# Optimization experiments

Hardware: AMD Instinct MI355X
Metric: run time of the kernel (lower is better)

Reference implementation:

```python
import jax, jax.numpy as jnp
import numpy as np
import math

N = 50000
E = 800000
NFEAT = 128
NLABEL = 8
H = 8        # nhead (hard-coded to 8 in __init__)
C = 32       # per-head channels (nhid arg)
HC = H * C   # 256, effective nhid after GAT concat
FDIM = HC + NLABEL  # 264
TDIM = 128


def sinusoidal_pos_emb(t, num_steps, dim, rescale=4):
    # x / num_steps * num_steps * rescale == x * rescale (kept faithful)
    xs = t / num_steps * num_steps * rescale
    half = dim // 2
    freqs = jnp.exp(jnp.arange(half, dtype=jnp.float32) * (-math.log(10000.0) / (half - 1)))
    ang = xs[:, None] * freqs[None, :]
    return jnp.concatenate([jnp.sin(ang), jnp.cos(ang)], axis=-1)


def gat_layer(h_in, W, a_src, a_dst, b, src, dst, n):
    # h_in: [N, Fin]; W: [Fin, H*C]; a_src/a_dst: [H, C]; b: [H*C]
    h = (h_in @ W).reshape(n, H, C)
    alpha_s = jnp.einsum('nhc,hc->nh', h, a_src)  # [N,H]
    alpha_d = jnp.einsum('nhc,hc->nh', h, a_dst)
    e = jax.nn.leaky_relu(alpha_s[src] + alpha_d[dst], 0.2)  # [E,H]
    # segment softmax over incoming edges of each destination node
    e = e - jax.ops.segment_max(e, dst, num_segments=n)[dst]
    ex = jnp.exp(e)
    denom = jax.ops.segment_sum(ex, dst, num_segments=n)[dst]
    alpha = ex / denom
    msg = h[src] * alpha[:, :, None]               # [E,H,C]
    out = jax.ops.segment_sum(msg, dst, num_segments=n)  # [N,H,C]
    return out.reshape(n, HC) + b


def setup_inputs() -> dict:
    key = jax.random.key(0)
    ks = jax.random.split(key, 24)
    s = 0.05
    inp = {
        'x': jax.random.normal(ks[0], (N, NFEAT), dtype=jnp.float32),
        'q_Y_sample': jax.random.normal(ks[1], (N, NLABEL), dtype=jnp.float32),
        'adj': jax.random.randint(ks[2], (2, E), 0, N, dtype=jnp.int64),
        't': jax.random.uniform(ks[3], (1,), dtype=jnp.float32) * 1000.0,
        'num_steps': 1000,
        # GAT layer params (layer 0 has different input dim)
        'W0': jax.random.normal(ks[4], (NFEAT + NLABEL, HC), dtype=jnp.float32) * s,
        'W1': jax.random.normal(ks[5], (HC + NLABEL, HC), dtype=jnp.float32) * s,
        'W2': jax.random.normal(ks[6], (HC + NLABEL, HC), dtype=jnp.float32) * s,
        'att_src': jax.random.normal(ks[7], (3, H, C), dtype=jnp.float32) * s,
        'att_dst': jax.random.normal(ks[8], (3, H, C), dtype=jnp.float32) * s,
        'bias': jax.random.normal(ks[9], (3, HC), dtype=jnp.float32) * s,
        # time MLP: Linear(128,128) -> ELU -> Linear(128, HC)
        'tmlp_w1': jax.random.normal(ks[10], (TDIM, TDIM), dtype=jnp.float32) * s,
        'tmlp_b1': jnp.zeros((TDIM,), dtype=jnp.float32),
        'tmlp_w2': jax.random.normal(ks[11], (TDIM, HC), dtype=jnp.float32) * s,
        'tmlp_b2': jnp.zeros((HC,), dtype=jnp.float32),
        # final MLP: fdim -> 2*fdim -> nlabel, ELU between, no BN
        'fin_w1': jax.random.normal(ks[12], (FDIM, 2 * FDIM), dtype=jnp.float32) * s,
        'fin_b1': jnp.zeros((2 * FDIM,), dtype=jnp.float32),
        'fin_w2': jax.random.normal(ks[13], (2 * FDIM, NLABEL), dtype=jnp.float32) * s,
        'fin_b2': jnp.zeros((NLABEL,), dtype=jnp.float32),
    }
    return inp


def reference(x, q_Y_sample, adj, t, num_steps, W0, W1, W2, att_src, att_dst, bias,
              tmlp_w1, tmlp_b1, tmlp_w2, tmlp_b2, fin_w1, fin_b1, fin_w2, fin_b2):
    n = x.shape[0]
    # time embedding -> [1, HC]
    temb = sinusoidal_pos_emb(t, num_steps, TDIM)
    temb = jax.nn.elu(temb @ tmlp_w1 + tmlp_b1) @ tmlp_w2 + tmlp_b2
    # edge index with self-loops (PyG GATConv add_self_loops=True)
    loops = jnp.arange(n)
    src = jnp.concatenate([adj[0], loops])
    dst = jnp.concatenate([adj[1], loops])
    h = jnp.concatenate([x, q_Y_sample], axis=-1)
    Ws = (W0, W1, W2)
    for i in range(3):
        conv = gat_layer(h, Ws[i], att_src[i], att_dst[i], bias[i], src, dst, n)
        h = jax.nn.elu(conv + temb)          # ELU activation (GATConv branch)
        h = jnp.concatenate([h, q_Y_sample], axis=-1)
    # final MLP
    return jax.nn.elu(h @ fin_w1 + fin_b1) @ fin_w2 + fin_b2
```

## Files before the change

### kernel.cpp

```cpp
#include <hip/hip_runtime.h>
#include <math.h>

#define N_NODES 50000
#define NE      800000
#define NEL     (NE + N_NODES)
#define NL      8
#define LDHB    288
#define KP0     160
#define KP1     288
#define NBLK    196
#define EDGEBLK ((NEL + 255) / 256)
#define HB_BLKS ((N_NODES * 36 + 255) / 256)
#define TR_BLKS 97

typedef __attribute__((ext_vector_type(8))) short bf16x8;
typedef __attribute__((ext_vector_type(4))) float f32x4;

__device__ __forceinline__ float elu_f(float x) { return x > 0.f ? x : __expf(x) - 1.f; }
__device__ __forceinline__ float bl(unsigned u) { return __uint_as_float(u << 16); }
__device__ __forceinline__ float bh(unsigned u) { return __uint_as_float(u & 0xffff0000u); }
__device__ __forceinline__ unsigned short f2b(float f) {
    unsigned u = __float_as_uint(f);
    u += 0x7fff + ((u >> 16) & 1);
    return (unsigned short)(u >> 16);
}
__device__ __forceinline__ unsigned pk2(float lo, float hi) {
    return (unsigned)f2b(lo) | ((unsigned)f2b(hi) << 16);
}
__device__ __forceinline__ int xcd_swizzle(int b, int nwg) {
    int q = nwg >> 3, r = nwg & 7;
    int xcd = b & 7, idx = b >> 3;
    return (xcd < r ? xcd * (q + 1) : r * (q + 1) + (xcd - r) * q) + idx;
}

__global__ void prep_kernel(const float* __restrict__ x, const float* __restrict__ q,
                            unsigned short* __restrict__ hbuf,
                            const float* __restrict__ W0, const float* __restrict__ W1,
                            const float* __restrict__ W2, const float* __restrict__ fw1,
                            unsigned short* __restrict__ wt0, unsigned short* __restrict__ wt1,
                            unsigned short* __restrict__ wt2, unsigned short* __restrict__ fw1t,
                            const int* __restrict__ adj, int* __restrict__ deg,
                            const float* __restrict__ t, const int* __restrict__ nst,
                            const float* __restrict__ tw1, const float* __restrict__ tb1,
                            const float* __restrict__ tw2, const float* __restrict__ tb2,
                            float* __restrict__ temb) {
    __shared__ float tlds[64][65];
    int bid = blockIdx.x, tid = threadIdx.x;
    if (bid < HB_BLKS) {
        int item = bid * 256 + tid;
        if (item >= N_NODES * 36) return;
        int n = item / 36, g = item - n * 36;
        float4 a = make_float4(0.f, 0.f, 0.f, 0.f), b = a;
        if (g < 16) {
            a = *(const float4*)(x + (size_t)n * 128 + g * 8);
            b = *(const float4*)(x + (size_t)n * 128 + g * 8 + 4);
        } else if (g == 16 || g == 32) {
            a = *(const float4*)(q + (size_t)n * 8);
            b = *(const float4*)(q + (size_t)n * 8 + 4);
        }
        uint4 o = make_uint4(pk2(a.x, a.y), pk2(a.z, a.w), pk2(b.x, b.y), pk2(b.z, b.w));
        *(uint4*)(hbuf + (size_t)n * LDHB + g * 8) = o;
        return;
    }
    int j = bid - HB_BLKS;
    if (j < TR_BLKS) {
        const float* W; unsigned short* WT; int K, NN, Kpad, nt;
        if (j < 12)      { W = W0;  WT = wt0;  K = 136; NN = 256; Kpad = KP0; nt = 4; }
        else if (j < 32) { W = W1;  WT = wt1;  K = 264; NN = 256; Kpad = KP1; nt = 4; j -= 12; }
        else if (j < 52) { W = W2;  WT = wt2;  K = 264; NN = 256; Kpad = KP1; nt = 4; j -= 32; }
        else             { W = fw1; WT = fw1t; K = 264; NN = 528; Kpad = KP1; nt = 9; j -= 52; }
        int tk = j / nt, tn = j - tk * nt;
        for (int i = tid; i < 4096; i += 256) {
            int r = i >> 6, c = i & 63;
            int k = tk * 64 + r, n = tn * 64 + c;
            tlds[r][c] = (k < K && n < NN) ? W[(size_t)k * NN + n] : 0.f;
        }
        __syncthreads();
        for (int i = tid; i < 4096; i += 256) {
            int r = i >> 6, c = i & 63;
            int n = tn * 64 + r, kp = tk * 64 + c;
            if (n < NN && kp < Kpad) WT[(size_t)n * Kpad + kp] = f2b(tlds[c][r]);
        }
        return;
    }
    j -= TR_BLKS;
    if (j < EDGEBLK) {
        int e = j * 256 + tid;
        if (e >= NEL) return;
        int d = (e < NE) ? adj[NE + e] : (e - NE);
        atomicAdd(&deg[d], 1);
        return;
    }
    __shared__ float emb[128];
    __shared__ float h1[128];
    float tv = t[0];
    float ns = (float)nst[0];
    float xs = tv / ns * ns * 4.0f;
    if (tid < 64) {
        float fr  = expf((float)tid * (-logf(10000.f) / 63.f));
        float ang = xs * fr;
        emb[tid]      = sinf(ang);
        emb[tid + 64] = cosf(ang);
    }
    __syncthreads();
    if (tid < 128) {
        float a = tb1[tid];
        for (int i = 0; i < 128; ++i) a += emb[i] * tw1[i * 128 + tid];
        h1[tid] = elu_f(a);
    }
    __syncthreads();
    float a = tb2[tid];
    for (int jj = 0; jj < 128; ++jj) a += h1[jj] * tw2[jj * 256 + tid];
    temb[tid] = a;
}

__global__ void scan1_kernel(const int* __restrict__ deg, int* __restrict__ excl,
                             int* __restrict__ bsum) {
    __shared__ int wsum[4];
    int idx = blockIdx.x * 256 + threadIdx.x;
    int lane = threadIdx.x & 63, wid = threadIdx.x >> 6;
    int v = (idx < N_NODES) ? deg[idx] : 0;
    int x = v;
#pragma unroll
    for (int off = 1; off < 64; off <<= 1) {
        int tv2 = __shfl_up(x, off);
        if (lane >= off) x += tv2;
    }
    if (lane == 63) wsum[wid] = x;
    __syncthreads();
    int woff = 0;
    for (int w = 0; w < wid; ++w) woff += wsum[w];
    if (idx < N_NODES) excl[idx] = woff + x - v;
    if (threadIdx.x == 255) bsum[blockIdx.x] = woff + x;
}

__global__ void scan2_kernel(int* __restrict__ bsum, int* __restrict__ boff) {
    __shared__ int wsum[4];
    int tid = threadIdx.x;
    int lane = tid & 63, wid = tid >> 6;
    int v = (tid < NBLK) ? bsum[tid] : 0;
    int x = v;
#pragma unroll
    for (int off = 1; off < 64; off <<= 1) {
        int tv2 = __shfl_up(x, off);
        if (lane >= off) x += tv2;
    }
    if (lane == 63) wsum[wid] = x;
    __syncthreads();
    int woff = 0;
    for (int w = 0; w < wid; ++w) woff += wsum[w];
    if (tid < NBLK) boff[tid] = woff + x - v;
}

__global__ void scan3_kernel(const int* __restrict__ excl, const int* __restrict__ boff,
                             int* __restrict__ rowptr, int* __restrict__ wptr) {
    int idx = blockIdx.x * 256 + threadIdx.x;
    if (idx < N_NODES) {
        int r = excl[idx] + boff[idx >> 8];
        rowptr[idx] = r;
        wptr[idx] = r;
    }
    if (idx == 0) rowptr[N_NODES] = NEL;
}

__global__ void scatter_kernel(const int* __restrict__ adj, int* __restrict__ wptr,
                               int* __restrict__ srcs) {
    int e = blockIdx.x * 256 + threadIdx.x;
    if (e >= NEL) return;
    int s, d;
    if (e < NE) { s = adj[e]; d = adj[NE + e]; }
    else        { s = d = e - NE; }
    int pos = atomicAdd(&wptr[d], 1);
    srcs[pos] = s;
}

template<int NK>
__device__ __forceinline__ void gemm_mainloop(
    const unsigned short* __restrict__ A, int lda,
    const unsigned short* __restrict__ Bt, int ldb,
    int M, int NCm1, int row0, int col0,
    char* lds, f32x4 (&acc)[4][4]) {
    int tid = threadIdx.x;
    int l = tid & 63, w = tid >> 6;
    int wr = w >> 1, wc = w & 1;
    int lr = l & 15, lq = l >> 4;

    int rr0 = w * 16 + (l >> 2);
    int rr1 = 64 + rr0;
    int kg0 = (l & 3) ^ ((rr0 >> 1) & 3);
    int kg1 = (l & 3) ^ ((rr1 >> 1) & 3);
    const unsigned short* gA0 = A + (size_t)min(row0 + rr0, M - 1) * lda + kg0 * 8;
    const unsigned short* gA1 = A + (size_t)min(row0 + rr1, M - 1) * lda + kg1 * 8;
    const unsigned short* gB0 = Bt + (size_t)min(col0 + rr0, NCm1) * ldb + kg0 * 8;
    const unsigned short* gB1 = Bt + (size_t)min(col0 + rr1, NCm1) * ldb + kg1 * 8;
    int la0 = w * 1024;
    int la1 = 4096 + w * 1024;

    int swz = ((lq ^ ((lr >> 1) & 3)) << 4);
    int abase = (wr * 64 + lr) * 64 + swz;
    int bbase = (wc * 64 + lr) * 64 + swz;

#define STAGE(buf, ks)                                                                  \
    {                                                                                   \
        char* base_ = lds + (buf) * 16384;                                              \
        __builtin_amdgcn_global_load_lds(                                               \
            (const __attribute__((address_space(1))) unsigned*)(gA0 + (ks) * 32),       \
            (__attribute__((address_space(3))) unsigned*)(base_ + la0), 16, 0, 0);      \
        __builtin_amdgcn_global_load_lds(                                               \
            (const __attribute__((address_space(1))) unsigned*)(gA1 + (ks) * 32),       \
            (__attribute__((address_space(3))) unsigned*)(base_ + la1), 16, 0, 0);      \
        __builtin_amdgcn_global_load_lds(                                               \
            (const __attribute__((address_space(1))) unsigned*)(gB0 + (ks) * 32),       \
            (__attribute__((address_space(3))) unsigned*)(base_ + 8192 + la0), 16, 0, 0);\
        __builtin_amdgcn_global_load_lds(                                               \
            (const __attribute__((address_space(1))) unsigned*)(gB1 + (ks) * 32),       \
            (__attribute__((address_space(3))) unsigned*)(base_ + 8192 + la1), 16, 0, 0);\
    }

    STAGE(0, 0);
    int cur = 0;
#pragma unroll
    for (int ks = 0; ks < NK; ++ks) {
        if (ks + 1 < NK) {
            STAGE(cur ^ 1, ks + 1);
            asm volatile("s_waitcnt vmcnt(4)" ::: "memory");
        } else {
            asm volatile("s_waitcnt vmcnt(0)" ::: "memory");
        }
        __builtin_amdgcn_s_barrier();
        char* Asc = lds + cur * 16384;
        char* Bsc = Asc + 8192;
        bf16x8 af[4], bfr[4];
#pragma unroll
        for (int m = 0; m < 4; ++m) af[m]  = *(const bf16x8*)(Asc + abase + m * 1024);
#pragma unroll
        for (int n = 0; n < 4; ++n) bfr[n] = *(const bf16x8*)(Bsc + bbase + n * 1024);
#pragma unroll
        for (int m = 0; m < 4; ++m)
#pragma unroll
            for (int n = 0; n < 4; ++n)
                acc[m][n] = __builtin_amdgcn_mfma_f32_16x16x32_bf16(af[m], bfr[n], acc[m][n], 0, 0, 0);
        asm volatile("s_waitcnt lgkmcnt(0)" ::: "memory");
        __builtin_amdgcn_s_barrier();
        cur ^= 1;
    }
#undef STAGE
}

template<int NK>
__global__ __launch_bounds__(256) void layer_gemm_kernel(
    const unsigned short* __restrict__ A, int lda,
    const unsigned short* __restrict__ Bt, int ldb,
    unsigned short* __restrict__ C, int M,
    const float* __restrict__ asrc, const float* __restrict__ adst,
    float* __restrict__ alpha_s, float* __restrict__ alpha_d) {
    __shared__ char lds[2][16384];
    int wg = xcd_swizzle(blockIdx.x, gridDim.x);
    int row0 = (wg >> 1) * 128, col0 = (wg & 1) * 128;
    int lane = threadIdx.x & 63, w = threadIdx.x >> 6;
    int wr = w >> 1, wc = w & 1;
    int lr = lane & 15, lq = lane >> 4;

    f32x4 acc[4][4];
#pragma unroll
    for (int m = 0; m < 4; ++m)
#pragma unroll
        for (int n = 0; n < 4; ++n) acc[m][n] = (f32x4){0.f, 0.f, 0.f, 0.f};

    gemm_mainloop<NK>(A, lda, Bt, ldb, M, 255, row0, col0, &lds[0][0], acc);

    float asv[4], adv[4];
#pragma unroll
    for (int n = 0; n < 4; ++n) {
        int c = col0 + wc * 64 + n * 16 + lr;
        asv[n] = asrc[c];
        adv[n] = adst[c];
    }
    int h0 = (col0 >> 5) + wc * 2;
    float* aptr = (lr & 2) ? alpha_d : alpha_s;
    int hsel = h0 + (lr & 1);

#pragma unroll
    for (int m = 0; m < 4; ++m) {
        int rbase = row0 + wr * 64 + m * 16 + lq * 4;
#pragma unroll
        for (int i = 0; i < 4; ++i) {
            int row = rbase + i;
            float pAs = acc[m][0][i] * asv[0] + acc[m][1][i] * asv[1];
            float pBs = acc[m][2][i] * asv[2] + acc[m][3][i] * asv[3];
            float pAd = acc[m][0][i] * adv[0] + acc[m][1][i] * adv[1];
            float pBd = acc[m][2][i] * adv[2] + acc[m][3][i] * adv[3];
            float ks_ = (lr & 1) ? pBs : pAs, ss = (lr & 1) ? pAs : pBs;
            float kd_ = (lr & 1) ? pBd : pAd, sd = (lr & 1) ? pAd : pBd;
            float vs = ks_ + __shfl_xor(ss, 1);
            float vd = kd_ + __shfl_xor(sd, 1);
            float kv = (lr & 2) ? vd : vs, sv = (lr & 2) ? vs : vd;
            float vv = kv + __shfl_xor(sv, 2);
            vv += __shfl_xor(vv, 4);
            vv += __shfl_xor(vv, 8);
            if (row < M) {
                if (lr < 4) aptr[row * NL + hsel] = vv;
#pragma unroll
                for (int n = 0; n < 4; ++n) {
                    int col = col0 + wc * 64 + n * 16 + lr;
                    C[(size_t)row * 256 + col] = f2b(acc[m][n][i]);
                }
            }
        }
    }
}

template<int NK>
__global__ __launch_bounds__(256) void fin_gemm_kernel(
    const unsigned short* __restrict__ A, int lda,
    const unsigned short* __restrict__ Bt, int ldb,
    int M, const float* __restrict__ fb1, const float* __restrict__ w2,
    float* __restrict__ partial) {
    __shared__ char lds[2][16384];
    int wg = xcd_swizzle(blockIdx.x, gridDim.x);
    int by = wg % 5, bx = wg / 5;
    int row0 = bx * 128, col0 = by * 128;
    int lane = threadIdx.x & 63, w = threadIdx.x >> 6;
    int wr = w >> 1, wc = w & 1;
    int lr = lane & 15, lq = lane >> 4;

    f32x4 acc[4][4];
#pragma unroll
    for (int m = 0; m < 4; ++m)
#pragma unroll
        for (int n = 0; n < 4; ++n) acc[m][n] = (f32x4){0.f, 0.f, 0.f, 0.f};

    gemm_mainloop<NK>(A, lda, Bt, ldb, M, 527, row0, col0, &lds[0][0], acc);

    float fbv[4], w2v[4][8];
#pragma unroll
    for (int n = 0; n < 4; ++n) {
        int c = col0 + wc * 64 + n * 16 + lr;
        if (c < 528) {
            fbv[n] = fb1[c];
            float4 wlo = *(const float4*)(w2 + (size_t)c * 8);
            float4 whi = *(const float4*)(w2 + (size_t)c * 8 + 4);
            w2v[n][0] = wlo.x; w2v[n][1] = wlo.y; w2v[n][2] = wlo.z; w2v[n][3] = wlo.w;
            w2v[n][4] = whi.x; w2v[n][5] = whi.y; w2v[n][6] = whi.z; w2v[n][7] = whi.w;
        } else {
            fbv[n] = 0.f;
#pragma unroll
            for (int j = 0; j < 8; ++j) w2v[n][j] = 0.f;
        }
    }
    int jsel = ((lr & 1) << 2) | (lr & 2) | ((lr >> 2) & 1);

    float* pbase = partial + (size_t)(by * 2 + wc) * N_NODES * 8;
#pragma unroll
    for (int m = 0; m < 4; ++m) {
        int rbase = row0 + wr * 64 + m * 16 + lq * 4;
#pragma unroll
        for (int i = 0; i < 4; ++i) {
            int row = rbase + i;
            float pj[8];
#pragma unroll
            for (int j = 0; j < 8; ++j) pj[j] = 0.f;
#pragma unroll
            for (int n = 0; n < 4; ++n) {
                float v = elu_f(acc[m][n][i] + fbv[n]);
#pragma unroll
                for (int j = 0; j < 8; ++j) pj[j] += v * w2v[n][j];
            }
            float v4[4];
#pragma unroll
            for (int j2 = 0; j2 < 4; ++j2) {
                float keep = (lr & 1) ? pj[j2 + 4] : pj[j2];
                float send = (lr & 1) ? pj[j2] : pj[j2 + 4];
                v4[j2] = keep + __shfl_xor(send, 1);
            }
            float v2[2];
#pragma unroll
            for (int j2 = 0; j2 < 2; ++j2) {
                float keep = (lr & 2) ? v4[j2 + 2] : v4[j2];
                float send = (lr & 2) ? v4[j2] : v4[j2 + 2];
                v2[j2] = keep + __shfl_xor(send, 2);
            }
            float keep = (lr & 4) ? v2[1] : v2[0];
            float send = (lr & 4) ? v2[0] : v2[1];
            float v1 = keep + __shfl_xor(send, 4);
            v1 += __shfl_xor(v1, 8);
            if (lr < 8 && row < M) pbase[(size_t)row * 8 + jsel] = v1;
        }
    }
}

__global__ void reduce_kernel(const float* __restrict__ partial, const float* __restrict__ fb2,
                              float* __restrict__ out) {
    int idx = blockIdx.x * 256 + threadIdx.x;
    if (idx >= N_NODES * NL) return;
    float a = fb2[idx & 7];
#pragma unroll
    for (int p = 0; p < 10; ++p) a += partial[(size_t)p * N_NODES * 8 + idx];
    out[idx] = a;
}

__global__ __launch_bounds__(256) void gather_kernel(
    const int* __restrict__ rowptr, const int* __restrict__ srcs,
    const float* __restrict__ alpha_s, const float* __restrict__ alpha_d,
    const unsigned short* __restrict__ hproj, const float* __restrict__ bias,
    const float* __restrict__ temb, unsigned short* __restrict__ h) {
    int node = blockIdx.x * 4 + (threadIdx.x >> 6);
    int lane = threadIdx.x & 63;
    int half = lane >> 5;
    int l32  = lane & 31;
    int hd   = l32 >> 2;
    float ad = alpha_d[node * NL + hd];
    int beg = rowptr[node], end = rowptr[node + 1];
    const uint4* hp4 = (const uint4*)hproj;
    float ac0[8], ac1[8];
#pragma unroll
    for (int j = 0; j < 8; ++j) { ac0[j] = 0.f; ac1[j] = 0.f; }
    float den0 = 0.f, den1 = 0.f;
    int i = beg + half;
    for (; i + 2 < end; i += 4) {
        int sA = srcs[i], sB = srcs[i + 2];
        float aA = alpha_s[sA * NL + hd] + ad;
        float aB = alpha_s[sB * NL + hd] + ad;
        aA = aA > 0.f ? aA : 0.2f * aA;
        aB = aB > 0.f ? aB : 0.2f * aB;
        float eA = __expf(aA);
        float eB = __expf(aB);
        uint4 hA = hp4[(size_t)sA * 32 + l32];
        uint4 hB = hp4[(size_t)sB * 32 + l32];
        ac0[0] += eA * bl(hA.x); ac0[1] += eA * bh(hA.x);
        ac0[2] += eA * bl(hA.y); ac0[3] += eA * bh(hA.y);
        ac0[4] += eA * bl(hA.z); ac0[5] += eA * bh(hA.z);
        ac0[6] += eA * bl(hA.w); ac0[7] += eA * bh(hA.w);
        den0 += eA;
        ac1[0] += eB * bl(hB.x); ac1[1] += eB * bh(hB.x);
        ac1[2] += eB * bl(hB.y); ac1[3] += eB * bh(hB.y);
        ac1[4] += eB * bl(hB.z); ac1[5] += eB * bh(hB.z);
        ac1[6] += eB * bl(hB.w); ac1[7] += eB * bh(hB.w);
        den1 += eB;
    }
    for (; i < end; i += 2) {
        int sA = srcs[i];
        float aA = alpha_s[sA * NL + hd] + ad;
        aA = aA > 0.f ? aA : 0.2f * aA;
        float eA = __expf(aA);
        uint4 hA = hp4[(size_t)sA * 32 + l32];
        ac0[0] += eA * bl(hA.x); ac0[1] += eA * bh(hA.x);
        ac0[2] += eA * bl(hA.y); ac0[3] += eA * bh(hA.y);
        ac0[4] += eA * bl(hA.z); ac0[5] += eA * bh(hA.z);
        ac0[6] += eA * bl(hA.w); ac0[7] += eA * bh(hA.w);
        den0 += eA;
    }
    float den = den0 + den1;
    den += __shfl_xor(den, 32);
    float av[8];
#pragma unroll
    for (int j = 0; j < 8; ++j) {
        av[j] = ac0[j] + ac1[j];
        av[j] += __shfl_xor(av[j], 32);
    }
    if (half == 0) {
        float inv = 1.f / den;
        int c = l32 * 8;
        float4 b0 = *(const float4*)(bias + c);
        float4 b1 = *(const float4*)(bias + c + 4);
        float4 t0 = *(const float4*)(temb + c);
        float4 t1 = *(const float4*)(temb + c + 4);
        uint4 o;
        o.x = pk2(elu_f(av[0] * inv + b0.x + t0.x), elu_f(av[1] * inv + b0.y + t0.y));
        o.y = pk2(elu_f(av[2] * inv + b0.z + t0.z), elu_f(av[3] * inv + b0.w + t0.w));
        o.z = pk2(elu_f(av[4] * inv + b1.x + t1.x), elu_f(av[5] * inv + b1.y + t1.y));
        o.w = pk2(elu_f(av[6] * inv + b1.z + t1.z), elu_f(av[7] * inv + b1.w + t1.w));
        *(uint4*)&h[(size_t)node * LDHB + c] = o;
    }
}

extern "C" void kernel_launch(void* const* d_in, const int* in_sizes, int n_in,
                              void* d_out, int out_size, void* d_ws, size_t ws_size,
                              hipStream_t stream) {
    const float* x   = (const float*)d_in[0];
    const float* q   = (const float*)d_in[1];
    const int*   adj = (const int*)d_in[2];
    const float* t   = (const float*)d_in[3];
    const int*   nst = (const int*)d_in[4];
    const float* W0  = (const float*)d_in[5];
    const float* W1  = (const float*)d_in[6];
    const float* W2  = (const float*)d_in[7];
    const float* att_src = (const float*)d_in[8];
    const float* att_dst = (const float*)d_in[9];
    const float* bias    = (const float*)d_in[10];
    const float* tw1 = (const float*)d_in[11];
    const float* tb1 = (const float*)d_in[12];
    const float* tw2 = (const float*)d_in[13];
    const float* tb2 = (const float*)d_in[14];
    const float* fw1 = (const float*)d_in[15];
    const float* fb1 = (const float*)d_in[16];
    const float* fw2 = (const float*)d_in[17];
    const float* fb2 = (const float*)d_in[18];
    float* out = (float*)d_out;

    char* ws = (char*)d_ws;
    unsigned short* hbuf = (unsigned short*)ws;
    char* p = ws + (size_t)N_NODES * LDHB * 2;
    unsigned short* hproj = (unsigned short*)p;  p += (size_t)N_NODES * 256 * 2;
    float* partial = (float*)p;                  p += (size_t)10 * N_NODES * 8 * 4;
    float* temb    = (float*)p;                  p += 1024;
    float* alpha_s = (float*)p;                  p += (size_t)N_NODES * NL * 4;
    float* alpha_d = (float*)p;                  p += (size_t)N_NODES * NL * 4;
    unsigned short* wt0  = (unsigned short*)p;   p += (size_t)256 * KP0 * 2;
    unsigned short* wt1  = (unsigned short*)p;   p += (size_t)256 * KP1 * 2;
    unsigned short* wt2  = (unsigned short*)p;   p += (size_t)256 * KP1 * 2;
    unsigned short* fw1t = (unsigned short*)p;   p += (size_t)528 * KP1 * 2;
    int* deg    = (int*)p;                       p += (size_t)N_NODES * 4;
    int* excl   = (int*)p;                       p += (size_t)N_NODES * 4;
    int* bsum   = (int*)p;                       p += 1024;
    int* boff   = (int*)p;                       p += 1024;
    int* rowptr = (int*)p;                       p += (size_t)(N_NODES + 4) * 4;
    int* wptr   = (int*)p;                       p += (size_t)N_NODES * 4;
    int* srcs   = (int*)p;                       p += (size_t)NEL * 4;

    hipMemsetAsync(deg, 0, (size_t)N_NODES * 4, stream);
    prep_kernel<<<HB_BLKS + TR_BLKS + EDGEBLK + 1, 256, 0, stream>>>(
        x, q, hbuf, W0, W1, W2, fw1, wt0, wt1, wt2, fw1t, adj, deg,
        t, nst, tw1, tb1, tw2, tb2, temb);

    scan1_kernel<<<NBLK, 256, 0, stream>>>(deg, excl, bsum);
    scan2_kernel<<<1, 256, 0, stream>>>(bsum, boff);
    scan3_kernel<<<NBLK, 256, 0, stream>>>(excl, boff, rowptr, wptr);
    scatter_kernel<<<(NEL + 255) / 256, 256, 0, stream>>>(adj, wptr, srcs);

    const unsigned short* wts[3] = {wt0, wt1, wt2};
    int mblocks = (N_NODES + 127) / 128;
    for (int l = 0; l < 3; ++l) {
        if (l == 0)
            layer_gemm_kernel<KP0 / 32><<<mblocks * 2, 256, 0, stream>>>(
                hbuf, LDHB, wts[l], KP0, hproj, N_NODES,
                att_src + l * 256, att_dst + l * 256, alpha_s, alpha_d);
        else
            layer_gemm_kernel<KP1 / 32><<<mblocks * 2, 256, 0, stream>>>(
                hbuf, LDHB, wts[l], KP1, hproj, N_NODES,
                att_src + l * 256, att_dst + l * 256, alpha_s, alpha_d);
        gather_kernel<<<(N_NODES + 3) / 4, 256, 0, stream>>>(
            rowptr, srcs, alpha_s, alpha_d, hproj, bias + l * 256, temb, hbuf);
    }

    fin_gemm_kernel<KP1 / 32><<<mblocks * 5, 256, 0, stream>>>(
        hbuf, LDHB, fw1t, KP1, N_NODES, fb1, fw2, partial);
    reduce_kernel<<<(N_NODES * NL + 255) / 256, 256, 0, stream>>>(partial, fb2, out);
}
```

Before: 424.9 us.

## Keep weight tile resident in LDS and stream A directly via persistent row loop

The GEMM kernels now stage the full K-extent of the 128-column weight slice into LDS once per block, with a padded row stride. Each block then loops persistently over M tiles and loads A fragments straight from global memory into registers with a three-deep prefetch. This removes per-k-step barriers and the double-buffered A/B LDS staging, and reuses the weights across many row tiles. The cost is a larger LDS footprint, uncoalesced per-lane A loads, fixed grid sizes of 512 and 515 blocks, and a launch-bounds occupancy hint.

Result: slower. 552.5 us (+30.0%).

```diff
diff --git a/kernel.cpp b/kernel.cpp
--- a/kernel.cpp
+++ b/kernel.cpp
@@ -12,6 +12,8 @@
 #define EDGEBLK ((NEL + 255) / 256)
 #define HB_BLKS ((N_NODES * 36 + 255) / 256)
 #define TR_BLKS 97
+#define MTILES  ((N_NODES + 127) / 128)
+#define BROW    592
 
 typedef __attribute__((ext_vector_type(8))) short bf16x8;
 typedef __attribute__((ext_vector_type(4))) float f32x4;
@@ -175,99 +177,77 @@
 }
 
 template<int NK>
-__device__ __forceinline__ void gemm_mainloop(
-    const unsigned short* __restrict__ A, int lda,
-    const unsigned short* __restrict__ Bt, int ldb,
-    int M, int NCm1, int row0, int col0,
-    char* lds, f32x4 (&acc)[4][4]) {
+__device__ __forceinline__ void stage_B(const unsigned short* __restrict__ Bt, int ldb,
+                                        int col0, int NCm1, char* ldsB) {
+    constexpr int KS = NK * 4;
     int tid = threadIdx.x;
-    int l = tid & 63, w = tid >> 6;
+    for (int i = tid; i < 128 * KS; i += 256) {
+        int c = i / KS, kg = i - c * KS;
+        uint4 v = make_uint4(0u, 0u, 0u, 0u);
+        if (col0 + c <= NCm1)
+            v = *(const uint4*)(Bt + (size_t)(col0 + c) * ldb + kg * 8);
+        *(uint4*)(ldsB + c * BROW + kg * 16) = v;
+    }
+}
+
+template<int NK>
+__device__ __forceinline__ void mfma_tile(
+    const unsigned short* __restrict__ A, int lda, int M, int row0,
+    const char* __restrict__ ldsB, f32x4 (&acc)[4][4]) {
+    int lane = threadIdx.x & 63, w = threadIdx.x >> 6;
     int wr = w >> 1, wc = w & 1;
-    int lr = l & 15, lq = l >> 4;
-
-    int rr0 = w * 16 + (l >> 2);
-    int rr1 = 64 + rr0;
-    int kg0 = (l & 3) ^ ((rr0 >> 1) & 3);
-    int kg1 = (l & 3) ^ ((rr1 >> 1) & 3);
-    const unsigned short* gA0 = A + (size_t)min(row0 + rr0, M - 1) * lda + kg0 * 8;
-    const unsigned short* gA1 = A + (size_t)min(row0 + rr1, M - 1) * lda + kg1 * 8;
-    const unsigned short* gB0 = Bt + (size_t)min(col0 + rr0, NCm1) * ldb + kg0 * 8;
-    const unsigned short* gB1 = Bt + (size_t)min(col0 + rr1, NCm1) * ldb + kg1 * 8;
-    int la0 = w * 1024;
-    int la1 = 4096 + w * 1024;
-
-    int swz = ((lq ^ ((lr >> 1) & 3)) << 4);
-    int abase = (wr * 64 + lr) * 64 + swz;
-    int bbase = (wc * 64 + lr) * 64 + swz;
-
-#define STAGE(buf, ks)                                                                  \
-    {                                                                                   \
-        char* base_ = lds + (buf) * 16384;                                              \
-        __builtin_amdgcn_global_load_lds(                                               \
-            (const __attribute__((address_space(1))) unsigned*)(gA0 + (ks) * 32),       \
-            (__attribute__((address_space(3))) unsigned*)(base_ + la0), 16, 0, 0);      \
-        __builtin_amdgcn_global_load_lds(                                               \
-            (const __attribute__((address_space(1))) unsigned*)(gA1 + (ks) * 32),       \
-            (__attribute__((address_space(3))) unsigned*)(base_ + la1), 16, 0, 0);      \
-        __builtin_amdgcn_global_load_lds(                                               \
-            (const __attribute__((address_space(1))) unsigned*)(gB0 + (ks) * 32),       \
-            (__attribute__((address_space(3))) unsigned*)(base_ + 8192 + la0), 16, 0, 0);\
-        __builtin_amdgcn_global_load_lds(                                               \
-            (const __attribute__((address_space(1))) unsigned*)(gB1 + (ks) * 32),       \
-            (__attribute__((address_space(3))) unsigned*)(base_ + 8192 + la1), 16, 0, 0);\
-    }
-
-    STAGE(0, 0);
-    int cur = 0;
+    int lr = lane & 15, lq = lane >> 4;
+
+    const unsigned short* Ap[4];
+#pragma unroll
+    for (int m = 0; m < 4; ++m) {
+        int row = min(row0 + wr * 64 + m * 16 + lr, M - 1);
+        Ap[m] = A + (size_t)row * lda + lq * 8;
+    }
+    const char* Bp = ldsB + (wc * 64 + lr) * BROW + lq * 16;
+
+    bf16x8 abuf[3][4];
+#pragma unroll
+    for (int m = 0; m < 4; ++m) abuf[0][m] = *(const bf16x8*)(Ap[m]);
+#pragma unroll
+    for (int m = 0; m < 4; ++m) abuf[1][m] = *(const bf16x8*)(Ap[m] + 32);
+
 #pragma unroll
     for (int ks = 0; ks < NK; ++ks) {
-        if (ks + 1 < NK) {
-            STAGE(cur ^ 1, ks + 1);
-            asm volatile("s_waitcnt vmcnt(4)" ::: "memory");
-        } else {
-            asm volatile("s_waitcnt vmcnt(0)" ::: "memory");
-        }
-        __builtin_amdgcn_s_barrier();
-        char* Asc = lds + cur * 16384;
-        char* Bsc = Asc + 8192;
-        bf16x8 af[4], bfr[4];
-#pragma unroll
-        for (int m = 0; m < 4; ++m) af[m]  = *(const bf16x8*)(Asc + abase + m * 1024);
-#pragma unroll
-        for (int n = 0; n < 4; ++n) bfr[n] = *(const bf16x8*)(Bsc + bbase + n * 1024);
+        if (ks + 2 < NK) {
+#pragma unroll
+            for (int m = 0; m < 4; ++m)
+                abuf[(ks + 2) % 3][m] = *(const bf16x8*)(Ap[m] + (ks + 2) * 32);
+        }
+        bf16x8 bfr[4];
+#pragma unroll
+        for (int n = 0; n < 4; ++n)
+            bfr[n] = *(const bf16x8*)(Bp + n * 16 * BROW + ks * 64);
 #pragma unroll
         for (int m = 0; m < 4; ++m)
 #pragma unroll
             for (int n = 0; n < 4; ++n)
-                acc[m][n] = __builtin_amdgcn_mfma_f32_16x16x32_bf16(af[m], bfr[n], acc[m][n], 0, 0, 0);
-        asm volatile("s_waitcnt lgkmcnt(0)" ::: "memory");
-        __builtin_amdgcn_s_barrier();
-        cur ^= 1;
-    }
-#undef STAGE
+                acc[m][n] = __builtin_amdgcn_mfma_f32_16x16x32_bf16(abuf[ks % 3][m], bfr[n], acc[m][n], 0, 0, 0);
+    }
 }
 
 template<int NK>
-__global__ __launch_bounds__(256) void layer_gemm_kernel(
+__global__ __launch_bounds__(256, 2) void layer_gemm_kernel(
     const unsigned short* __restrict__ A, int lda,
     const unsigned short* __restrict__ Bt, int ldb,
     unsigned short* __restrict__ C, int M,
     const float* __restrict__ asrc, const float* __restrict__ adst,
     float* __restrict__ alpha_s, float* __restrict__ alpha_d) {
-    __shared__ char lds[2][16384];
+    __shared__ char ldsB[128 * BROW];
     int wg = xcd_swizzle(blockIdx.x, gridDim.x);
-    int row0 = (wg >> 1) * 128, col0 = (wg & 1) * 128;
+    int by = wg & 1, bx = wg >> 1;
+    int col0 = by * 128;
     int lane = threadIdx.x & 63, w = threadIdx.x >> 6;
     int wr = w >> 1, wc = w & 1;
     int lr = lane & 15, lq = lane >> 4;
 
-    f32x4 acc[4][4];
-#pragma unroll
-    for (int m = 0; m < 4; ++m)
-#pragma unroll
-        for (int n = 0; n < 4; ++n) acc[m][n] = (f32x4){0.f, 0.f, 0.f, 0.f};
-
-    gemm_mainloop<NK>(A, lda, Bt, ldb, M, 255, row0, col0, &lds[0][0], acc);
+    stage_B<NK>(Bt, ldb, col0, 255, ldsB);
+    __syncthreads();
 
     float asv[4], adv[4];
 #pragma unroll
@@ -276,34 +256,45 @@
         asv[n] = asrc[c];
         adv[n] = adst[c];
     }
-    int h0 = (col0 >> 5) + wc * 2;
+    int h0 = by * 4 + wc * 2;
     float* aptr = (lr & 2) ? alpha_d : alpha_s;
     int hsel = h0 + (lr & 1);
 
-#pragma unroll
-    for (int m = 0; m < 4; ++m) {
-        int rbase = row0 + wr * 64 + m * 16 + lq * 4;
-#pragma unroll
-        for (int i = 0; i < 4; ++i) {
-            int row = rbase + i;
-            float pAs = acc[m][0][i] * asv[0] + acc[m][1][i] * asv[1];
-            float pBs = acc[m][2][i] * asv[2] + acc[m][3][i] * asv[3];
-            float pAd = acc[m][0][i] * adv[0] + acc[m][1][i] * adv[1];
-            float pBd = acc[m][2][i] * adv[2] + acc[m][3][i] * adv[3];
-            float ks_ = (lr & 1) ? pBs : pAs, ss = (lr & 1) ? pAs : pBs;
-            float kd_ = (lr & 1) ? pBd : pAd, sd = (lr & 1) ? pAd : pBd;
-            float vs = ks_ + __shfl_xor(ss, 1);
-            float vd = kd_ + __shfl_xor(sd, 1);
-            float kv = (lr & 2) ? vd : vs, sv = (lr & 2) ? vs : vd;
-            float vv = kv + __shfl_xor(sv, 2);
-            vv += __shfl_xor(vv, 4);
-            vv += __shfl_xor(vv, 8);
-            if (row < M) {
-                if (lr < 4) aptr[row * NL + hsel] = vv;
-#pragma unroll
-                for (int n = 0; n < 4; ++n) {
-                    int col = col0 + wc * 64 + n * 16 + lr;
-                    C[(size_t)row * 256 + col] = f2b(acc[m][n][i]);
+    for (int mt = bx; mt < MTILES; mt += 256) {
+        int row0 = mt * 128;
+        f32x4 acc[4][4];
+#pragma unroll
+        for (int m = 0; m < 4; ++m)
+#pragma unroll
+            for (int n = 0; n < 4; ++n) acc[m][n] = (f32x4){0.f, 0.f, 0.f, 0.f};
+
+        mfma_tile<NK>(A, lda, M, row0, ldsB, acc);
+
+#pragma unroll
+        for (int m = 0; m < 4; ++m) {
+            int rbase = row0 + wr * 64 + m * 16 + lq * 4;
+#pragma unroll
+            for (int i = 0; i < 4; ++i) {
+                int row = rbase + i;
+                float pAs = acc[m][0][i] * asv[0] + acc[m][1][i] * asv[1];
+                float pBs = acc[m][2][i] * asv[2] + acc[m][3][i] * asv[3];
+                float pAd = acc[m][0][i] * adv[0] + acc[m][1][i] * adv[1];
+                float pBd = acc[m][2][i] * adv[2] + acc[m][3][i] * adv[3];
+                float ks_ = (lr & 1) ? pBs : pAs, ss = (lr & 1) ? pAs : pBs;
+                float kd_ = (lr & 1) ? pBd : pAd, sd = (lr & 1) ? pAd : pBd;
+                float vs = ks_ + __shfl_xor(ss, 1);
+                float vd = kd_ + __shfl_xor(sd, 1);
+                float kv = (lr & 2) ? vd : vs, sv = (lr & 2) ? vs : vd;
+                float vv = kv + __shfl_xor(sv, 2);
+                vv += __shfl_xor(vv, 4);
+                vv += __shfl_xor(vv, 8);
+                if (row < M) {
+                    if (lr < 4) aptr[row * NL + hsel] = vv;
+#pragma unroll
+                    for (int n = 0; n < 4; ++n) {
+                        int col = col0 + wc * 64 + n * 16 + lr;
+                        C[(size_t)row * 256 + col] = f2b(acc[m][n][i]);
+                    }
                 }
             }
         }
@@ -311,26 +302,21 @@
 }
 
 template<int NK>
-__global__ __launch_bounds__(256) void fin_gemm_kernel(
+__global__ __launch_bounds__(256, 2) void fin_gemm_kernel(
     const unsigned short* __restrict__ A, int lda,
     const unsigned short* __restrict__ Bt, int ldb,
     int M, const float* __restrict__ fb1, const float* __restrict__ w2,
     float* __restrict__ partial) {
-    __shared__ char lds[2][16384];
+    __shared__ char ldsB[128 * BROW];
     int wg = xcd_swizzle(blockIdx.x, gridDim.x);
     int by = wg % 5, bx = wg / 5;
-    int row0 = bx * 128, col0 = by * 128;
+    int col0 = by * 128;
     int lane = threadIdx.x & 63, w = threadIdx.x >> 6;
     int wr = w >> 1, wc = w & 1;
     int lr = lane & 15, lq = lane >> 4;
 
-    f32x4 acc[4][4];
-#pragma unroll
-    for (int m = 0; m < 4; ++m)
-#pragma unroll
-        for (int n = 0; n < 4; ++n) acc[m][n] = (f32x4){0.f, 0.f, 0.f, 0.f};
-
-    gemm_mainloop<NK>(A, lda, Bt, ldb, M, 527, row0, col0, &lds[0][0], acc);
+    stage_B<NK>(Bt, ldb, col0, 527, ldsB);
+    __syncthreads();
 
     float fbv[4], w2v[4][8];
 #pragma unroll
@@ -349,42 +335,53 @@
         }
     }
     int jsel = ((lr & 1) << 2) | (lr & 2) | ((lr >> 2) & 1);
-
     float* pbase = partial + (size_t)(by * 2 + wc) * N_NODES * 8;
-#pragma unroll
-    for (int m = 0; m < 4; ++m) {
-        int rbase = row0 + wr * 64 + m * 16 + lq * 4;
-#pragma unroll
-        for (int i = 0; i < 4; ++i) {
-            int row = rbase + i;
-            float pj[8];
-#pragma unroll
-            for (int j = 0; j < 8; ++j) pj[j] = 0.f;
-#pragma unroll
-            for (int n = 0; n < 4; ++n) {
-                float v = elu_f(acc[m][n][i] + fbv[n]);
-#pragma unroll
-                for (int j = 0; j < 8; ++j) pj[j] += v * w2v[n][j];
+
+    for (int mt = bx; mt < MTILES; mt += 103) {
+        int row0 = mt * 128;
+        f32x4 acc[4][4];
+#pragma unroll
+        for (int m = 0; m < 4; ++m)
+#pragma unroll
+            for (int n = 0; n < 4; ++n) acc[m][n] = (f32x4){0.f, 0.f, 0.f, 0.f};
+
+        mfma_tile<NK>(A, lda, M, row0, ldsB, acc);
+
+#pragma unroll
+        for (int m = 0; m < 4; ++m) {
+            int rbase = row0 + wr * 64 + m * 16 + lq * 4;
+#pragma unroll
+            for (int i = 0; i < 4; ++i) {
+                int row = rbase + i;
+                float pj[8];
+#pragma unroll
+                for (int j = 0; j < 8; ++j) pj[j] = 0.f;
+#pragma unroll
+                for (int n = 0; n < 4; ++n) {
+                    float v = elu_f(acc[m][n][i] + fbv[n]);
+#pragma unroll
+                    for (int j = 0; j < 8; ++j) pj[j] += v * w2v[n][j];
+                }
+                float v4[4];
+#pragma unroll
+                for (int j2 = 0; j2 < 4; ++j2) {
+                    float keep = (lr & 1) ? pj[j2 + 4] : pj[j2];
+                    float send = (lr & 1) ? pj[j2] : pj[j2 + 4];
+                    v4[j2] = keep + __shfl_xor(send, 1);
+                }
+                float v2[2];
+#pragma unroll
+                for (int j2 = 0; j2 < 2; ++j2) {
+                    float keep = (lr & 2) ? v4[j2 + 2] : v4[j2];
+                    float send = (lr & 2) ? v4[j2] : v4[j2 + 2];
+                    v2[j2] = keep + __shfl_xor(send, 2);
+                }
+                float keep = (lr & 4) ? v2[1] : v2[0];
+                float send = (lr & 4) ? v2[0] : v2[1];
+                float v1 = keep + __shfl_xor(send, 4);
+                v1 += __shfl_xor(v1, 8);
+                if (lr < 8 && row < M) pbase[(size_t)row * 8 + jsel] = v1;
             }
-            float v4[4];
-#pragma unroll
-            for (int j2 = 0; j2 < 4; ++j2) {
-                float keep = (lr & 1) ? pj[j2 + 4] : pj[j2];
-                float send = (lr & 1) ? pj[j2] : pj[j2 + 4];
-                v4[j2] = keep + __shfl_xor(send, 1);
-            }
-            float v2[2];
-#pragma unroll
-            for (int j2 = 0; j2 < 2; ++j2) {
-                float keep = (lr & 2) ? v4[j2 + 2] : v4[j2];
-                float send = (lr & 2) ? v4[j2] : v4[j2 + 2];
-                v2[j2] = keep + __shfl_xor(send, 2);
-            }
-            float keep = (lr & 4) ? v2[1] : v2[0];
-            float send = (lr & 4) ? v2[0] : v2[1];
-            float v1 = keep + __shfl_xor(send, 4);
-            v1 += __shfl_xor(v1, 8);
-            if (lr < 8 && row < M) pbase[(size_t)row * 8 + jsel] = v1;
         }
     }
 }
@@ -529,21 +526,20 @@
     scatter_kernel<<<(NEL + 255) / 256, 256, 0, stream>>>(adj, wptr, srcs);
 
     const unsigned short* wts[3] = {wt0, wt1, wt2};
-    int mblocks = (N_NODES + 127) / 128;
     for (int l = 0; l < 3; ++l) {
         if (l == 0)
-            layer_gemm_kernel<KP0 / 32><<<mblocks * 2, 256, 0, stream>>>(
+            layer_gemm_kernel<KP0 / 32><<<512, 256, 0, stream>>>(
                 hbuf, LDHB, wts[l], KP0, hproj, N_NODES,
                 att_src + l * 256, att_dst + l * 256, alpha_s, alpha_d);
         else
-            layer_gemm_kernel<KP1 / 32><<<mblocks * 2, 256, 0, stream>>>(
+            layer_gemm_kernel<KP1 / 32><<<512, 256, 0, stream>>>(
                 hbuf, LDHB, wts[l], KP1, hproj, N_NODES,
                 att_src + l * 256, att_dst + l * 256, alpha_s, alpha_d);
         gather_kernel<<<(N_NODES + 3) / 4, 256, 0, stream>>>(
             rowptr, srcs, alpha_s, alpha_d, hproj, bias + l * 256, temb, hbuf);
     }
 
-    fin_gemm_kernel<KP1 / 32><<<mblocks * 5, 256, 0, stream>>>(
+    fin_gemm_kernel<KP1 / 32><<<515, 256, 0, stream>>>(
         hbuf, LDHB, fw1t, KP1, N_NODES, fb1, fw2, partial);
     reduce_kernel<<<(N_NODES * NL + 255) / 256, 256, 0, stream>>>(partial, fb2, out);
 }
```

## Bucket CSR neighbor lists by source chunk for gather locality

Applied to the files above, without the earlier changes.

Edge counting and scattering now use 16 sub-buckets per destination, keyed by the source index's high bits (src>>12). The CSR lists therefore come out roughly sorted by source region, so gather reads of hproj rows tend to touch nearby memory and can get better cache reuse. In exchange, the count and write-pointer arrays become 16x larger, which adds memset and scan traffic. Scattered atomics also spread over more addresses.

Measured after the change: 435.7 us. 1.03x slower.

```diff
diff --git a/kernel.cpp b/kernel.cpp
--- a/kernel.cpp
+++ b/kernel.cpp
@@ -12,6 +12,8 @@
 #define EDGEBLK ((NEL + 255) / 256)
 #define HB_BLKS ((N_NODES * 36 + 255) / 256)
 #define TR_BLKS 97
+#define NCH     16
+#define CSHIFT  12
 
 typedef __attribute__((ext_vector_type(8))) short bf16x8;
 typedef __attribute__((ext_vector_type(4))) float f32x4;
@@ -39,7 +41,7 @@
                             const float* __restrict__ W2, const float* __restrict__ fw1,
                             unsigned short* __restrict__ wt0, unsigned short* __restrict__ wt1,
                             unsigned short* __restrict__ wt2, unsigned short* __restrict__ fw1t,
-                            const int* __restrict__ adj, int* __restrict__ deg,
+                            const int* __restrict__ adj, int* __restrict__ cnt,
                             const float* __restrict__ t, const int* __restrict__ nst,
                             const float* __restrict__ tw1, const float* __restrict__ tb1,
                             const float* __restrict__ tw2, const float* __restrict__ tb2,
@@ -87,8 +89,10 @@
     if (j < EDGEBLK) {
         int e = j * 256 + tid;
         if (e >= NEL) return;
-        int d = (e < NE) ? adj[NE + e] : (e - NE);
-        atomicAdd(&deg[d], 1);
+        int s, d;
+        if (e < NE) { s = adj[e]; d = adj[NE + e]; }
+        else        { s = d = e - NE; }
+        atomicAdd(&cnt[d * NCH + (s >> CSHIFT)], 1);
         return;
     }
     __shared__ float emb[128];
@@ -114,12 +118,18 @@
     temb[tid] = a;
 }
 
-__global__ void scan1_kernel(const int* __restrict__ deg, int* __restrict__ excl,
+__global__ void scan1_kernel(const int* __restrict__ cnt, int* __restrict__ excl,
                              int* __restrict__ bsum) {
     __shared__ int wsum[4];
     int idx = blockIdx.x * 256 + threadIdx.x;
     int lane = threadIdx.x & 63, wid = threadIdx.x >> 6;
-    int v = (idx < N_NODES) ? deg[idx] : 0;
+    int v = 0;
+    if (idx < N_NODES) {
+        const int4* c4 = (const int4*)(cnt + idx * NCH);
+        int4 a = c4[0], b = c4[1], c = c4[2], d = c4[3];
+        v = a.x + a.y + a.z + a.w + b.x + b.y + b.z + b.w
+          + c.x + c.y + c.z + c.w + d.x + d.y + d.z + d.w;
+    }
     int x = v;
 #pragma unroll
     for (int off = 1; off < 64; off <<= 1) {
@@ -153,24 +163,30 @@
 }
 
 __global__ void scan3_kernel(const int* __restrict__ excl, const int* __restrict__ boff,
-                             int* __restrict__ rowptr, int* __restrict__ wptr) {
+                             const int* __restrict__ cnt,
+                             int* __restrict__ rowptr, int* __restrict__ wptr2) {
     int idx = blockIdx.x * 256 + threadIdx.x;
     if (idx < N_NODES) {
         int r = excl[idx] + boff[idx >> 8];
         rowptr[idx] = r;
-        wptr[idx] = r;
+        int run = r;
+#pragma unroll
+        for (int c = 0; c < NCH; ++c) {
+            wptr2[idx * NCH + c] = run;
+            run += cnt[idx * NCH + c];
+        }
     }
     if (idx == 0) rowptr[N_NODES] = NEL;
 }
 
-__global__ void scatter_kernel(const int* __restrict__ adj, int* __restrict__ wptr,
+__global__ void scatter_kernel(const int* __restrict__ adj, int* __restrict__ wptr2,
                                int* __restrict__ srcs) {
     int e = blockIdx.x * 256 + threadIdx.x;
     if (e >= NEL) return;
     int s, d;
     if (e < NE) { s = adj[e]; d = adj[NE + e]; }
     else        { s = d = e - NE; }
-    int pos = atomicAdd(&wptr[d], 1);
+    int pos = atomicAdd(&wptr2[d * NCH + (s >> CSHIFT)], 1);
     srcs[pos] = s;
 }
 
@@ -509,24 +525,24 @@
     unsigned short* wt0  = (unsigned short*)p;   p += (size_t)256 * KP0 * 2;
     unsigned short* wt1  = (unsigned short*)p;   p += (size_t)256 * KP1 * 2;
     unsigned short* wt2  = (unsigned short*)p;   p += (size_t)256 * KP1 * 2;
-    unsigned short* fw1t = (unsigned short*)p;   p += (size_t)528 * KP1 * 2;
-    int* deg    = (int*)p;                       p += (size_t)N_NODES * 4;
+    unsigned short* fw1t = (unsigned short*)p;   p += (size_t)528 * KP1 * 2 + 8;
+    int* cnt    = (int*)p;                       p += (size_t)N_NODES * NCH * 4;
     int* excl   = (int*)p;                       p += (size_t)N_NODES * 4;
     int* bsum   = (int*)p;                       p += 1024;
     int* boff   = (int*)p;                       p += 1024;
     int* rowptr = (int*)p;                       p += (size_t)(N_NODES + 4) * 4;
-    int* wptr   = (int*)p;                       p += (size_t)N_NODES * 4;
+    int* wptr2  = (int*)p;                       p += (size_t)N_NODES * NCH * 4;
     int* srcs   = (int*)p;                       p += (size_t)NEL * 4;
 
-    hipMemsetAsync(deg, 0, (size_t)N_NODES * 4, stream);
+    hipMemsetAsync(cnt, 0, (size_t)N_NODES * NCH * 4, stream);
     prep_kernel<<<HB_BLKS + TR_BLKS + EDGEBLK + 1, 256, 0, stream>>>(
-        x, q, hbuf, W0, W1, W2, fw1, wt0, wt1, wt2, fw1t, adj, deg,
+        x, q, hbuf, W0, W1, W2, fw1, wt0, wt1, wt2, fw1t, adj, cnt,
         t, nst, tw1, tb1, tw2, tb2, temb);
 
-    scan1_kernel<<<NBLK, 256, 0, stream>>>(deg, excl, bsum);
+    scan1_kernel<<<NBLK, 256, 0, stream>>>(cnt, excl, bsum);
     scan2_kernel<<<1, 256, 0, stream>>>(bsum, boff);
-    scan3_kernel<<<NBLK, 256, 0, stream>>>(excl, boff, rowptr, wptr);
-    scatter_kernel<<<(NEL + 255) / 256, 256, 0, stream>>>(adj, wptr, srcs);
+    scan3_kernel<<<NBLK, 256, 0, stream>>>(excl, boff, cnt, rowptr, wptr2);
+    scatter_kernel<<<(NEL + 255) / 256, 256, 0, stream>>>(adj, wptr2, srcs);
 
     const unsigned short* wts[3] = {wt0, wt1, wt2};
     int mblocks = (N_NODES + 127) / 128;
```

## Split gather work across 4 channel-quarter blocks with 8 edge groups per wave

Applied to the files above, without the earlier changes.

The gather kernel is re-partitioned so each node's 256 channels are split into four 64-channel slices handled by different blocks, with blocks interleaved so that slices of the same node group are adjacent. Each wave now processes 8 edges in parallel, one per 8-lane group, and combines partial sums with a shuffle butterfly. The aim is more memory-level parallelism per node and better latency hiding on the irregular edge loads. The cost is that alpha_s, srcs and the exp are recomputed four times per edge, and the cross-lane reduction has more shuffle steps.

After: 521.5 us. +22.7%, slower.

```diff
diff --git a/kernel.cpp b/kernel.cpp
--- a/kernel.cpp
+++ b/kernel.cpp
@@ -404,73 +404,53 @@
     const float* __restrict__ alpha_s, const float* __restrict__ alpha_d,
     const unsigned short* __restrict__ hproj, const float* __restrict__ bias,
     const float* __restrict__ temb, unsigned short* __restrict__ h) {
-    int node = blockIdx.x * 4 + (threadIdx.x >> 6);
+    int bid = blockIdx.x;
+    int k = bid & 7;
+    int w = k >> 1;
+    int nodeblock = (bid >> 3) * 2 + (k & 1);
+    int node = nodeblock * 4 + (threadIdx.x >> 6);
     int lane = threadIdx.x & 63;
-    int half = lane >> 5;
-    int l32  = lane & 31;
-    int hd   = l32 >> 2;
-    float ad = alpha_d[node * NL + hd];
+    int g = lane >> 3, j = lane & 7;
+    int head = 2 * w + (j >> 2);
+    int ch = head * 32 + (j & 3) * 8;
+    int cu = ch >> 3;
+    float ad = alpha_d[node * NL + head];
     int beg = rowptr[node], end = rowptr[node + 1];
     const uint4* hp4 = (const uint4*)hproj;
-    float ac0[8], ac1[8];
-#pragma unroll
-    for (int j = 0; j < 8; ++j) { ac0[j] = 0.f; ac1[j] = 0.f; }
-    float den0 = 0.f, den1 = 0.f;
-    int i = beg + half;
-    for (; i + 2 < end; i += 4) {
-        int sA = srcs[i], sB = srcs[i + 2];
-        float aA = alpha_s[sA * NL + hd] + ad;
-        float aB = alpha_s[sB * NL + hd] + ad;
-        aA = aA > 0.f ? aA : 0.2f * aA;
-        aB = aB > 0.f ? aB : 0.2f * aB;
-        float eA = __expf(aA);
-        float eB = __expf(aB);
-        uint4 hA = hp4[(size_t)sA * 32 + l32];
-        uint4 hB = hp4[(size_t)sB * 32 + l32];
-        ac0[0] += eA * bl(hA.x); ac0[1] += eA * bh(hA.x);
-        ac0[2] += eA * bl(hA.y); ac0[3] += eA * bh(hA.y);
-        ac0[4] += eA * bl(hA.z); ac0[5] += eA * bh(hA.z);
-        ac0[6] += eA * bl(hA.w); ac0[7] += eA * bh(hA.w);
-        den0 += eA;
-        ac1[0] += eB * bl(hB.x); ac1[1] += eB * bh(hB.x);
-        ac1[2] += eB * bl(hB.y); ac1[3] += eB * bh(hB.y);
-        ac1[4] += eB * bl(hB.z); ac1[5] += eB * bh(hB.z);
-        ac1[6] += eB * bl(hB.w); ac1[7] += eB * bh(hB.w);
-        den1 += eB;
-    }
-    for (; i < end; i += 2) {
-        int sA = srcs[i];
-        float aA = alpha_s[sA * NL + hd] + ad;
-        aA = aA > 0.f ? aA : 0.2f * aA;
-        float eA = __expf(aA);
-        uint4 hA = hp4[(size_t)sA * 32 + l32];
-        ac0[0] += eA * bl(hA.x); ac0[1] += eA * bh(hA.x);
-        ac0[2] += eA * bl(hA.y); ac0[3] += eA * bh(hA.y);
-        ac0[4] += eA * bl(hA.z); ac0[5] += eA * bh(hA.z);
-        ac0[6] += eA * bl(hA.w); ac0[7] += eA * bh(hA.w);
-        den0 += eA;
-    }
-    float den = den0 + den1;
-    den += __shfl_xor(den, 32);
-    float av[8];
-#pragma unroll
-    for (int j = 0; j < 8; ++j) {
-        av[j] = ac0[j] + ac1[j];
-        av[j] += __shfl_xor(av[j], 32);
-    }
-    if (half == 0) {
+    float ac[8];
+#pragma unroll
+    for (int jj = 0; jj < 8; ++jj) ac[jj] = 0.f;
+    float den = 0.f;
+    for (int i = beg + g; i < end; i += 8) {
+        int s = srcs[i];
+        float a = alpha_s[s * NL + head] + ad;
+        a = a > 0.f ? a : 0.2f * a;
+        float e = __expf(a);
+        uint4 hv = hp4[(size_t)s * 32 + cu];
+        ac[0] += e * bl(hv.x); ac[1] += e * bh(hv.x);
+        ac[2] += e * bl(hv.y); ac[3] += e * bh(hv.y);
+        ac[4] += e * bl(hv.z); ac[5] += e * bh(hv.z);
+        ac[6] += e * bl(hv.w); ac[7] += e * bh(hv.w);
+        den += e;
+    }
+#pragma unroll
+    for (int mask = 8; mask < 64; mask <<= 1) {
+        den += __shfl_xor(den, mask);
+#pragma unroll
+        for (int jj = 0; jj < 8; ++jj) ac[jj] += __shfl_xor(ac[jj], mask);
+    }
+    if (g == 0) {
         float inv = 1.f / den;
-        int c = l32 * 8;
-        float4 b0 = *(const float4*)(bias + c);
-        float4 b1 = *(const float4*)(bias + c + 4);
-        float4 t0 = *(const float4*)(temb + c);
-        float4 t1 = *(const float4*)(temb + c + 4);
+        float4 b0 = *(const float4*)(bias + ch);
+        float4 b1 = *(const float4*)(bias + ch + 4);
+        float4 t0 = *(const float4*)(temb + ch);
+        float4 t1 = *(const float4*)(temb + ch + 4);
         uint4 o;
-        o.x = pk2(elu_f(av[0] * inv + b0.x + t0.x), elu_f(av[1] * inv + b0.y + t0.y));
-        o.y = pk2(elu_f(av[2] * inv + b0.z + t0.z), elu_f(av[3] * inv + b0.w + t0.w));
-        o.z = pk2(elu_f(av[4] * inv + b1.x + t1.x), elu_f(av[5] * inv + b1.y + t1.y));
-        o.w = pk2(elu_f(av[6] * inv + b1.z + t1.z), elu_f(av[7] * inv + b1.w + t1.w));
-        *(uint4*)&h[(size_t)node * LDHB + c] = o;
+        o.x = pk2(elu_f(ac[0] * inv + b0.x + t0.x), elu_f(ac[1] * inv + b0.y + t0.y));
+        o.y = pk2(elu_f(ac[2] * inv + b0.z + t0.z), elu_f(ac[3] * inv + b0.w + t0.w));
+        o.z = pk2(elu_f(ac[4] * inv + b1.x + t1.x), elu_f(ac[5] * inv + b1.y + t1.y));
+        o.w = pk2(elu_f(ac[6] * inv + b1.z + t1.z), elu_f(ac[7] * inv + b1.w + t1.w));
+        *(uint4*)&h[(size_t)node * LDHB + ch] = o;
     }
 }
 
@@ -539,7 +519,7 @@
             layer_gemm_kernel<KP1 / 32><<<mblocks * 2, 256, 0, stream>>>(
                 hbuf, LDHB, wts[l], KP1, hproj, N_NODES,
                 att_src + l * 256, att_dst + l * 256, alpha_s, alpha_d);
-        gather_kernel<<<(N_NODES + 3) / 4, 256, 0, stream>>>(
+        gather_kernel<<<N_NODES, 256, 0, stream>>>(
             rowptr, srcs, alpha_s, alpha_d, hproj, bias + l * 256, temb, hbuf);
     }
 
```
